# Kernel tuning notes

Hardware: AMD Instinct MI355X
Metric: run time of the kernel (lower is better)

## Reference

```python
import jax, jax.numpy as jnp
import numpy as np

N = 50000      # nodes
E = 800000     # edges (before self loops)
G = 64         # graphs in batch
F_IN = 11
HID = 64
C = 8
NEG_SLOPE = 0.2


def setup_inputs() -> dict:
    key = jax.random.key(0)
    ks = jax.random.split(key, 20)
    inp = {
        "x": jax.random.normal(ks[0], (N, F_IN), dtype=jnp.float32),
        "edge_index": jax.random.randint(ks[1], (2, E), 0, N, dtype=jnp.int64),
        "edge_attr": jax.random.normal(ks[2], (E, 17), dtype=jnp.float32),
        "batch": jnp.sort(jax.random.randint(ks[3], (N,), 0, G, dtype=jnp.int64)),
    }
    def glorot(k, shape):
        fan_in, fan_out = shape[0], shape[-1]
        s = jnp.sqrt(6.0 / (fan_in + fan_out))
        return jax.random.uniform(k, shape, jnp.float32, -s, s)
    # GATConv layers (heads=1): W [in,out], att vectors a_src/a_dst [out], bias [out]
    inp["W1"] = glorot(ks[4], (F_IN, HID)); inp["a1s"] = glorot(ks[5], (HID,)); inp["a1d"] = glorot(ks[6], (HID,)); inp["b1"] = jnp.zeros((HID,), jnp.float32)
    inp["W2"] = glorot(ks[7], (HID, HID)); inp["a2s"] = glorot(ks[8], (HID,)); inp["a2d"] = glorot(ks[9], (HID,)); inp["b2"] = jnp.zeros((HID,), jnp.float32)
    inp["W3"] = glorot(ks[10], (HID, C)); inp["a3s"] = glorot(ks[11], (C,)); inp["a3d"] = glorot(ks[12], (C,)); inp["b3"] = jnp.zeros((C,), jnp.float32)
    return inp


def _gat_layer(x, src, dst, W, a_s, a_d, b):
    # x: [N,in] -> h: [N,out]; single head, concat irrelevant for heads=1
    h = x @ W
    alpha_src = h @ a_s            # [N]
    alpha_dst = h @ a_d            # [N]
    e = jax.nn.leaky_relu(alpha_src[src] + alpha_dst[dst], negative_slope=NEG_SLOPE)  # [E']
    # segment-wise (per destination node) softmax over incoming edges
    m = jax.ops.segment_max(e, dst, num_segments=N)
    ex = jnp.exp(e - m[dst])
    denom = jax.ops.segment_sum(ex, dst, num_segments=N)
    alpha = ex / denom[dst]
    out = jax.ops.segment_sum(alpha[:, None] * h[src], dst, num_segments=N)
    return out + b


def reference(x, edge_index, edge_attr, batch, W1, a1s, a1d, b1, W2, a2s, a2d, b2, W3, a3s, a3d, b3):
    del edge_attr  # GATConv without edge_dim ignores edge_attr
    loop = jnp.arange(N, dtype=edge_index.dtype)
    src = jnp.concatenate([edge_index[0], loop])  # add self loops
    dst = jnp.concatenate([edge_index[1], loop])
    h = jax.nn.relu(_gat_layer(x, src, dst, W1, a1s, a1d, b1))
    h = jax.nn.relu(_gat_layer(h, src, dst, W2, a2s, a2d, b2))
    h = jax.nn.relu(_gat_layer(h, src, dst, W3, a3s, a3d, b3))
    # global mean pool over graphs
    counts = jax.ops.segment_sum(jnp.ones((N,), h.dtype), batch, num_segments=G)
    pooled = jax.ops.segment_sum(h, batch, num_segments=G) / jnp.maximum(counts, 1.0)[:, None]
    # dropout is identity in eval mode
    return jax.nn.sigmoid(pooled)
```

## Files before the change

kernel.cpp:

```cpp
#include <hip/hip_runtime.h>

#define NN 50000
#define EE 800000
#define GG 64
#define CC 8

#define NBKT 196
#define NCHK 782
#define CHUNK 1024
#define CAP 8192
#define NB4G 12500

__device__ unsigned g_done = 0;

__device__ __forceinline__ float lrelu(float z) { return fmaxf(z, 0.2f * z); }
__device__ __forceinline__ unsigned short f2bf(float v) {
    unsigned u = __float_as_uint(v);
    return (unsigned short)((u + 0x7FFFu + ((u >> 16) & 1u)) >> 16);
}
__device__ __forceinline__ float bf2f(unsigned short b) {
    return __uint_as_float(((unsigned)b) << 16);
}


__global__ __launch_bounds__(256) void k0_mm11_hist(const float* __restrict__ x, const float* __restrict__ W,
                                                    const float* __restrict__ avs, const float* __restrict__ avd,
                                                    unsigned short* __restrict__ h, float* __restrict__ as_,
                                                    float* __restrict__ ad_, const int* __restrict__ dst,
                                                    int* __restrict__ G) {
    __shared__ float xT[11 * 68];
    __shared__ float Wl[11 * 64];
    __shared__ float avl[64], adl[64];
    __shared__ int hist[NBKT];
    int t = threadIdx.x;
    int nbase = blockIdx.x * 64;
    for (int idx = t; idx < 11 * 64; idx += 256) Wl[idx] = W[idx];
    if (t < 64) { avl[t] = avs[t]; adl[t] = avd[t]; }
    for (int idx = t; idx < 64 * 11; idx += 256) {
        int n = idx / 11, k = idx - n * 11;
        int gn = nbase + n;
        if (gn >= NN) gn = NN - 1;
        xT[k * 68 + n] = x[gn * 11 + k];
    }
    for (int i = t; i < NBKT; i += 256) hist[i] = 0;
    __syncthreads();
    int f0 = (t & 15) * 4;
    int n0 = (t >> 4) * 4;
    float a00=0,a01=0,a02=0,a03=0, a10=0,a11=0,a12=0,a13=0;
    float a20=0,a21=0,a22=0,a23=0, a30=0,a31=0,a32=0,a33=0;
#pragma unroll
    for (int k = 0; k < 11; k++) {
        float4 xv = *(const float4*)&xT[k * 68 + n0];
        float4 wv = *(const float4*)&Wl[k * 64 + f0];
        a00 += xv.x * wv.x; a01 += xv.x * wv.y; a02 += xv.x * wv.z; a03 += xv.x * wv.w;
        a10 += xv.y * wv.x; a11 += xv.y * wv.y; a12 += xv.y * wv.z; a13 += xv.y * wv.w;
        a20 += xv.z * wv.x; a21 += xv.z * wv.y; a22 += xv.z * wv.z; a23 += xv.z * wv.w;
        a30 += xv.w * wv.x; a31 += xv.w * wv.y; a32 += xv.w * wv.z; a33 += xv.w * wv.w;
    }
    float4 av = *(const float4*)&avl[f0];
    float4 dv = *(const float4*)&adl[f0];
    float vs[4], vd[4];
    vs[0] = a00*av.x + a01*av.y + a02*av.z + a03*av.w;
    vs[1] = a10*av.x + a11*av.y + a12*av.z + a13*av.w;
    vs[2] = a20*av.x + a21*av.y + a22*av.z + a23*av.w;
    vs[3] = a30*av.x + a31*av.y + a32*av.z + a33*av.w;
    vd[0] = a00*dv.x + a01*dv.y + a02*dv.z + a03*dv.w;
    vd[1] = a10*dv.x + a11*dv.y + a12*dv.z + a13*dv.w;
    vd[2] = a20*dv.x + a21*dv.y + a22*dv.z + a23*dv.w;
    vd[3] = a30*dv.x + a31*dv.y + a32*dv.z + a33*dv.w;
#pragma unroll
    for (int o = 1; o < 16; o <<= 1) {
#pragma unroll
        for (int ni = 0; ni < 4; ni++) {
            vs[ni] += __shfl_xor(vs[ni], o);
            vd[ni] += __shfl_xor(vd[ni], o);
        }
    }
    ushort4* h4 = (ushort4*)h;
    int nn0 = nbase + n0;
    float rows[4][4] = {{a00,a01,a02,a03},{a10,a11,a12,a13},{a20,a21,a22,a23},{a30,a31,a32,a33}};
#pragma unroll
    for (int ni = 0; ni < 4; ni++) {
        if (nn0 + ni < NN) {
            ushort4 pv;
            pv.x = f2bf(rows[ni][0]); pv.y = f2bf(rows[ni][1]);
            pv.z = f2bf(rows[ni][2]); pv.w = f2bf(rows[ni][3]);
            h4[(nn0 + ni) * 16 + (t & 15)] = pv;
            if ((t & 15) == 0) { as_[nn0 + ni] = vs[ni]; ad_[nn0 + ni] = vd[ni]; }
        }
    }
    int e0 = blockIdx.x * CHUNK;
    int e1 = min(e0 + CHUNK, EE);
    for (int e = e0 + t; e < e1; e += 256) atomicAdd(&hist[dst[e] >> 8], 1);
    __syncthreads();
    for (int i = t; i < NBKT; i += 256) G[blockIdx.x * NBKT + i] = hist[i];
}


__global__ __launch_bounds__(256) void k1_scan(const int* __restrict__ G, int* __restrict__ offs,
                                               int* __restrict__ bT, float* __restrict__ pool,
                                               float* __restrict__ cntf, int* __restrict__ rowptr) {
    __shared__ int s[256];
    int t = threadIdx.x, j = blockIdx.x;
    int c0 = t * 4;
    int v0 = (c0 + 0 < NCHK) ? G[(c0 + 0) * NBKT + j] : 0;
    int v1 = (c0 + 1 < NCHK) ? G[(c0 + 1) * NBKT + j] : 0;
    int v2 = (c0 + 2 < NCHK) ? G[(c0 + 2) * NBKT + j] : 0;
    int v3 = (c0 + 3 < NCHK) ? G[(c0 + 3) * NBKT + j] : 0;
    int tsum = v0 + v1 + v2 + v3;
    s[t] = tsum;
    __syncthreads();
#pragma unroll
    for (int off = 1; off < 256; off <<= 1) {
        int u = (t >= off) ? s[t - off] : 0;
        __syncthreads();
        s[t] += u;
        __syncthreads();
    }
    int excl = s[t] - tsum;
    if (c0 + 0 < NCHK) offs[(c0 + 0) * NBKT + j] = excl;
    if (c0 + 1 < NCHK) offs[(c0 + 1) * NBKT + j] = excl + v0;
    if (c0 + 2 < NCHK) offs[(c0 + 2) * NBKT + j] = excl + v0 + v1;
    if (c0 + 3 < NCHK) offs[(c0 + 3) * NBKT + j] = excl + v0 + v1 + v2;
    if (t == 255) bT[j] = s[255];
    if (j == 0) {
        for (int i = t; i < GG * CC; i += 256) pool[i] = 0.f;
        if (t < GG) cntf[t] = 0.f;
        if (t == 0) rowptr[NN] = EE;
    }
}


__global__ __launch_bounds__(256) void k2_part(const int* __restrict__ src, const int* __restrict__ dst,
                                               const int* __restrict__ offs, const int* __restrict__ bT,
                                               unsigned* __restrict__ pairs) {
    __shared__ int s[256];
    __shared__ int bst[NBKT];
    __shared__ int cur[NBKT];
    int t = threadIdx.x, c = blockIdx.x;
    int v = (t < NBKT) ? bT[t] : 0;
    s[t] = v;
    __syncthreads();
#pragma unroll
    for (int off = 1; off < 256; off <<= 1) {
        int u = (t >= off) ? s[t - off] : 0;
        __syncthreads();
        s[t] += u;
        __syncthreads();
    }
    if (t < NBKT) bst[t] = s[t] - v;
    __syncthreads();
    for (int i = t; i < NBKT; i += 256) cur[i] = bst[i] + offs[c * NBKT + i];
    __syncthreads();
    int e0 = c * CHUNK, e1 = min(e0 + CHUNK, EE);
    for (int e = e0 + t; e < e1; e += 256) {
        int d = dst[e];
        int pos = atomicAdd(&cur[d >> 8], 1);
        pairs[pos] = (unsigned)src[e] | ((unsigned)(d & 255) << 16);
    }
}


__global__ __launch_bounds__(256) void k3_sort(const unsigned* __restrict__ pairs, const int* __restrict__ bT,
                                               int* __restrict__ col, int* __restrict__ rowptr) {
    __shared__ unsigned pL[CAP];
    __shared__ int hist[256];
    __shared__ int sc[256];
    int t = threadIdx.x, j = blockIdx.x;
    int v = (t < NBKT) ? bT[t] : 0;
    hist[t] = v;
    __syncthreads();
#pragma unroll
    for (int off = 1; off < 256; off <<= 1) {
        int u = (t >= off) ? hist[t - off] : 0;
        __syncthreads();
        hist[t] += u;
        __syncthreads();
    }
    if (t == j) { sc[0] = hist[t] - v; sc[1] = v; }
    __syncthreads();
    int start = sc[0];
    int cnt = sc[1];
    if (cnt > CAP) cnt = CAP;
    int nb = j * 256;
    int nodeCnt = min(256, NN - nb);
    __syncthreads();
    hist[t] = 0;
    __syncthreads();
    for (int i = t; i < cnt; i += 256) {
        unsigned p = pairs[start + i];
        pL[i] = p;
        atomicAdd(&hist[p >> 16], 1);
    }
    __syncthreads();
    int c2 = hist[t];
    sc[t] = c2;
    __syncthreads();
#pragma unroll
    for (int off = 1; off < 256; off <<= 1) {
        int u = (t >= off) ? sc[t - off] : 0;
        __syncthreads();
        sc[t] += u;
        __syncthreads();
    }
    int excl = sc[t] - c2;
    if (t < nodeCnt) rowptr[nb + t] = start + excl;
    hist[t] = excl;
    __syncthreads();
    for (int i = t; i < cnt; i += 256) {
        unsigned p = pL[i];
        int pos = atomicAdd(&hist[p >> 16], 1);
        col[start + pos] = (int)(p & 0xFFFFu);
    }
}


__global__ __launch_bounds__(256) void k_mm64t(const unsigned short* __restrict__ xin,
                                               const float* __restrict__ W,
                                               const float* __restrict__ avs, const float* __restrict__ avd,
                                               unsigned short* __restrict__ h, float* __restrict__ as_,
                                               float* __restrict__ ad_) {
    __shared__ float xT[64 * 68];
    __shared__ float Wl[64 * 64];
    __shared__ float avl[64], adl[64];
    int t = threadIdx.x;
    int nbase = blockIdx.x * 64;
    for (int idx = t; idx < 64 * 64; idx += 256) Wl[idx] = W[idx];
    if (t < 64) { avl[t] = avs[t]; adl[t] = avd[t]; }
    for (int idx = t; idx < 64 * 64; idx += 256) {
        int n = idx / 64, k = idx - n * 64;
        int gn = nbase + n;
        if (gn >= NN) gn = NN - 1;
        xT[k * 68 + n] = bf2f(xin[gn * 64 + k]);
    }
    __syncthreads();
    int f0 = (t & 15) * 4;
    int n0 = (t >> 4) * 4;
    float a00=0,a01=0,a02=0,a03=0, a10=0,a11=0,a12=0,a13=0;
    float a20=0,a21=0,a22=0,a23=0, a30=0,a31=0,a32=0,a33=0;
#pragma unroll 4
    for (int k = 0; k < 64; k++) {
        float4 xv = *(const float4*)&xT[k * 68 + n0];
        float4 wv = *(const float4*)&Wl[k * 64 + f0];
        a00 += xv.x * wv.x; a01 += xv.x * wv.y; a02 += xv.x * wv.z; a03 += xv.x * wv.w;
        a10 += xv.y * wv.x; a11 += xv.y * wv.y; a12 += xv.y * wv.z; a13 += xv.y * wv.w;
        a20 += xv.z * wv.x; a21 += xv.z * wv.y; a22 += xv.z * wv.z; a23 += xv.z * wv.w;
        a30 += xv.w * wv.x; a31 += xv.w * wv.y; a32 += xv.w * wv.z; a33 += xv.w * wv.w;
    }
    float4 av = *(const float4*)&avl[f0];
    float4 dv = *(const float4*)&adl[f0];
    float vs[4], vd[4];
    vs[0] = a00*av.x + a01*av.y + a02*av.z + a03*av.w;
    vs[1] = a10*av.x + a11*av.y + a12*av.z + a13*av.w;
    vs[2] = a20*av.x + a21*av.y + a22*av.z + a23*av.w;
    vs[3] = a30*av.x + a31*av.y + a32*av.z + a33*av.w;
    vd[0] = a00*dv.x + a01*dv.y + a02*dv.z + a03*dv.w;
    vd[1] = a10*dv.x + a11*dv.y + a12*dv.z + a13*dv.w;
    vd[2] = a20*dv.x + a21*dv.y + a22*dv.z + a23*dv.w;
    vd[3] = a30*dv.x + a31*dv.y + a32*dv.z + a33*dv.w;
#pragma unroll
    for (int o = 1; o < 16; o <<= 1) {
#pragma unroll
        for (int ni = 0; ni < 4; ni++) {
            vs[ni] += __shfl_xor(vs[ni], o);
            vd[ni] += __shfl_xor(vd[ni], o);
        }
    }
    ushort4* h4 = (ushort4*)h;
    int nn0 = nbase + n0;
    float rows[4][4] = {{a00,a01,a02,a03},{a10,a11,a12,a13},{a20,a21,a22,a23},{a30,a31,a32,a33}};
#pragma unroll
    for (int ni = 0; ni < 4; ni++) {
        if (nn0 + ni < NN) {
            ushort4 pv;
            pv.x = f2bf(rows[ni][0]); pv.y = f2bf(rows[ni][1]);
            pv.z = f2bf(rows[ni][2]); pv.w = f2bf(rows[ni][3]);
            h4[(nn0 + ni) * 16 + (t & 15)] = pv;
            if ((t & 15) == 0) { as_[nn0 + ni] = vs[ni]; ad_[nn0 + ni] = vd[ni]; }
        }
    }
}


template <bool FUSE>
__global__ __launch_bounds__(256) void k_agg64(const unsigned short* __restrict__ h,
                                               const int* __restrict__ rowptr,
                                               const int* __restrict__ col, const float* __restrict__ as_,
                                               const float* __restrict__ ad_, const float* __restrict__ bias,
                                               unsigned short* __restrict__ out16,
                                               const float* __restrict__ W3, const float* __restrict__ a3s,
                                               const float* __restrict__ a3d,
                                               float* __restrict__ as3, float* __restrict__ ad3) {
    __shared__ uint2 ws[4][64];
    __shared__ float W3p[64 * 10];
    if constexpr (FUSE) {
        for (int idx = threadIdx.x; idx < 512; idx += 256)
            W3p[(idx >> 3) * 10 + (idx & 7)] = W3[idx];
    }
    int wid = threadIdx.x >> 6;
    int node = blockIdx.x * 4 + wid;
    int lane = threadIdx.x & 63;
    int rp0 = rowptr[node];
    int deg = rowptr[node + 1] - rp0;
    float adn = ad_[node];
    float zself = lrelu(as_[node] + adn);
    const ushort4* hb = (const ushort4*)h;
    int f = lane & 15, eg = lane >> 4;
    float4 acc = make_float4(0.f, 0.f, 0.f, 0.f);
    if (deg <= 64) {
        int s = 0;
        float z = -1e30f;
        if (lane < deg) {
            s = col[rp0 + lane];
            z = lrelu(as_[s] + adn);
        }
        float M = z;
#pragma unroll
        for (int o = 32; o; o >>= 1) M = fmaxf(M, __shfl_xor(M, o));
        M = fmaxf(M, zself);
        float ex = (lane < deg) ? __expf(z - M) : 0.f;
        float exs = __expf(zself - M);
        float sum = ex;
#pragma unroll
        for (int o = 32; o; o >>= 1) sum += __shfl_xor(sum, o);
        float inv = 1.f / (sum + exs);
        float wl = ex * inv;
        ws[wid][lane] = make_uint2(__float_as_uint(wl), (unsigned)s);
        __syncthreads();
        const uint4* wsp = (const uint4*)&ws[wid][0];
        for (int base = 0; base < deg; base += 8) {
            uint4 p = wsp[(base >> 1) + eg];
            float wa = __uint_as_float(p.x);
            float wb = __uint_as_float(p.z);
            ushort4 ha = hb[p.y * 16 + f];
            ushort4 hc = hb[p.w * 16 + f];
            acc.x += wa * bf2f(ha.x) + wb * bf2f(hc.x);
            acc.y += wa * bf2f(ha.y) + wb * bf2f(hc.y);
            acc.z += wa * bf2f(ha.z) + wb * bf2f(hc.z);
            acc.w += wa * bf2f(ha.w) + wb * bf2f(hc.w);
        }
        if (eg == 0) {
            float w0 = exs * inv;
            ushort4 hv = hb[node * 16 + f];
            acc.x += w0 * bf2f(hv.x);
            acc.y += w0 * bf2f(hv.y);
            acc.z += w0 * bf2f(hv.z);
            acc.w += w0 * bf2f(hv.w);
        }
    } else {
        __syncthreads();
        float m = -1e30f, l = 0.f;
        for (int i = lane; i < deg; i += 64) {
            float z = lrelu(as_[col[rp0 + i]] + adn);
            float mn = fmaxf(m, z);
            l = l * __expf(m - mn) + __expf(z - mn);
            m = mn;
        }
        if (lane == 0) {
            float mn = fmaxf(m, zself);
            l = l * __expf(m - mn) + __expf(zself - mn);
            m = mn;
        }
#pragma unroll
        for (int o = 32; o; o >>= 1) {
            float mo = __shfl_xor(m, o), lo = __shfl_xor(l, o);
            float mn = fmaxf(m, mo);
            l = l * __expf(m - mn) + lo * __expf(mo - mn);
            m = mn;
        }
        float Em = m;
        float inv = 1.f / l;
        for (int base = 0; base < deg; base += 4) {
            int i = base + eg;
            if (i < deg) {
                int sv = col[rp0 + i];
                float al = __expf(lrelu(as_[sv] + adn) - Em) * inv;
                ushort4 hv = hb[sv * 16 + f];
                acc.x += al * bf2f(hv.x);
                acc.y += al * bf2f(hv.y);
                acc.z += al * bf2f(hv.z);
                acc.w += al * bf2f(hv.w);
            }
        }
        if (eg == 0) {
            float al = __expf(zself - Em) * inv;
            ushort4 hv = hb[node * 16 + f];
            acc.x += al * bf2f(hv.x);
            acc.y += al * bf2f(hv.y);
            acc.z += al * bf2f(hv.z);
            acc.w += al * bf2f(hv.w);
        }
    }
#pragma unroll
    for (int o = 16; o <= 32; o <<= 1) {
        acc.x += __shfl_xor(acc.x, o);
        acc.y += __shfl_xor(acc.y, o);
        acc.z += __shfl_xor(acc.z, o);
        acc.w += __shfl_xor(acc.w, o);
    }
    float4 bv = ((const float4*)bias)[f];
    float r0 = fmaxf(acc.x + bv.x, 0.f);
    float r1 = fmaxf(acc.y + bv.y, 0.f);
    float r2 = fmaxf(acc.z + bv.z, 0.f);
    float r3 = fmaxf(acc.w + bv.w, 0.f);
    if constexpr (!FUSE) {
        if (eg == 0) {
            ushort4 pv;
            pv.x = f2bf(r0); pv.y = f2bf(r1); pv.z = f2bf(r2); pv.w = f2bf(r3);
            ((ushort4*)out16)[node * 16 + f] = pv;
        }
    } else {
        int j0 = eg * 2;
        int kb = f * 4;
        float p0 = 0.f, p1 = 0.f;
#pragma unroll
        for (int i = 0; i < 4; i++) {
            float2 w = *(const float2*)&W3p[(kb + i) * 10 + j0];
            float rv = (i == 0) ? r0 : (i == 1) ? r1 : (i == 2) ? r2 : r3;
            p0 += rv * w.x;
            p1 += rv * w.y;
        }
#pragma unroll
        for (int o = 1; o < 16; o <<= 1) {
            p0 += __shfl_xor(p0, o);
            p1 += __shfl_xor(p1, o);
        }
        float vs = p0 * a3s[j0] + p1 * a3s[j0 + 1];
        float vd = p0 * a3d[j0] + p1 * a3d[j0 + 1];
        vs += __shfl_xor(vs, 16); vs += __shfl_xor(vs, 32);
        vd += __shfl_xor(vd, 16); vd += __shfl_xor(vd, 32);
        if (lane == 0) { as3[node] = vs; ad3[node] = vd; }
        if (f == 0) {
            ushort2 pv;
            pv.x = f2bf(p0); pv.y = f2bf(p1);
            ((ushort2*)out16)[node * 4 + eg] = pv;
        }
    }
}


__global__ __launch_bounds__(256) void k_agg8(const unsigned short* __restrict__ h,
                                              const int* __restrict__ rowptr,
                                              const int* __restrict__ col, const float* __restrict__ as_,
                                              const float* __restrict__ ad_, const float* __restrict__ bias,
                                              float* __restrict__ out) {
    __shared__ uint2 ws[4][64];
    int wid = threadIdx.x >> 6;
    int node = blockIdx.x * 4 + wid;
    int lane = threadIdx.x & 63;
    int rp0 = rowptr[node];
    int deg = rowptr[node + 1] - rp0;
    float adn = ad_[node];
    float zself = lrelu(as_[node] + adn);
    const ushort2* h2v = (const ushort2*)h;
    int f = lane & 3, eg = lane >> 2;
    float2 acc = make_float2(0.f, 0.f);
    if (deg <= 64) {
        int s = 0;
        float z = -1e30f;
        if (lane < deg) {
            s = col[rp0 + lane];
            z = lrelu(as_[s] + adn);
        }
        float M = z;
#pragma unroll
        for (int o = 32; o; o >>= 1) M = fmaxf(M, __shfl_xor(M, o));
        M = fmaxf(M, zself);
        float ex = (lane < deg) ? __expf(z - M) : 0.f;
        float exs = __expf(zself - M);
        float sum = ex;
#pragma unroll
        for (int o = 32; o; o >>= 1) sum += __shfl_xor(sum, o);
        float inv = 1.f / (sum + exs);
        float wl = ex * inv;
        ws[wid][lane] = make_uint2(__float_as_uint(wl), (unsigned)s);
        __syncthreads();
        const uint4* wsp = (const uint4*)&ws[wid][0];
        for (int base = 0; base < deg; base += 32) {
            uint4 p = wsp[(base >> 1) + eg];
            float wa = __uint_as_float(p.x);
            float wb = __uint_as_float(p.z);
            ushort2 ha = h2v[p.y * 4 + f];
            ushort2 hc = h2v[p.w * 4 + f];
            acc.x += wa * bf2f(ha.x) + wb * bf2f(hc.x);
            acc.y += wa * bf2f(ha.y) + wb * bf2f(hc.y);
        }
        if (eg == 0) {
            float w0 = exs * inv;
            ushort2 hv = h2v[node * 4 + f];
            acc.x += w0 * bf2f(hv.x);
            acc.y += w0 * bf2f(hv.y);
        }
    } else {
        __syncthreads();
        float m = -1e30f, l = 0.f;
        for (int i = lane; i < deg; i += 64) {
            float z = lrelu(as_[col[rp0 + i]] + adn);
            float mn = fmaxf(m, z);
            l = l * __expf(m - mn) + __expf(z - mn);
            m = mn;
        }
        if (lane == 0) {
            float mn = fmaxf(m, zself);
            l = l * __expf(m - mn) + __expf(zself - mn);
            m = mn;
        }
#pragma unroll
        for (int o = 32; o; o >>= 1) {
            float mo = __shfl_xor(m, o), lo = __shfl_xor(l, o);
            float mn = fmaxf(m, mo);
            l = l * __expf(m - mn) + lo * __expf(mo - mn);
            m = mn;
        }
        float Em = m;
        float inv = 1.f / l;
        for (int base = 0; base < deg; base += 16) {
            int i = base + eg;
            if (i < deg) {
                int sv = col[rp0 + i];
                float al = __expf(lrelu(as_[sv] + adn) - Em) * inv;
                ushort2 hv = h2v[sv * 4 + f];
                acc.x += al * bf2f(hv.x);
                acc.y += al * bf2f(hv.y);
            }
        }
        if (eg == 0) {
            float al = __expf(zself - Em) * inv;
            ushort2 hv = h2v[node * 4 + f];
            acc.x += al * bf2f(hv.x);
            acc.y += al * bf2f(hv.y);
        }
    }
#pragma unroll
    for (int o = 4; o <= 32; o <<= 1) {
        acc.x += __shfl_xor(acc.x, o);
        acc.y += __shfl_xor(acc.y, o);
    }
    if (eg == 0) {
        float2 bv = ((const float2*)bias)[f];
        float2 o2;
        o2.x = fmaxf(acc.x + bv.x, 0.f);
        o2.y = fmaxf(acc.y + bv.y, 0.f);
        ((float2*)out)[node * 4 + f] = o2;
    }
}


__global__ __launch_bounds__(256) void k9_poolfinal(const float* __restrict__ h3, const int* __restrict__ batch,
                                                    float* __restrict__ pool, float* __restrict__ cntf,
                                                    float* __restrict__ out) {
    __shared__ float pl[GG * CC + GG];
    __shared__ int lastFlag;
    int t = threadIdx.x;
    for (int idx = t; idx < GG * CC + GG; idx += 256) pl[idx] = 0.f;
    __syncthreads();
    int node = blockIdx.x * 256 + t;
    if (node < NN) {
        int g = batch[node];
#pragma unroll
        for (int c = 0; c < CC; c++) atomicAdd(&pl[g * CC + c], h3[node * CC + c]);
        atomicAdd(&pl[GG * CC + g], 1.0f);
    }
    __syncthreads();
    for (int idx = t; idx < GG * CC + GG; idx += 256) {
        float v = pl[idx];
        if (idx < GG * CC)
            atomicAdd(&pool[idx], v);
        else
            atomicAdd(&cntf[idx - GG * CC], v);
    }
    __syncthreads();
    if (t == 0) {
        __threadfence();
        unsigned r = __hip_atomic_fetch_add(&g_done, 1u, __ATOMIC_ACQ_REL, __HIP_MEMORY_SCOPE_AGENT);
        lastFlag = (r == (unsigned)(NBKT - 1));
    }
    __syncthreads();
    if (lastFlag) {
        __threadfence();
        for (int i = t; i < GG * CC; i += 256) {
            int g = i >> 3;
            float c = __hip_atomic_load(&cntf[g], __ATOMIC_RELAXED, __HIP_MEMORY_SCOPE_AGENT);
            float p = __hip_atomic_load(&pool[i], __ATOMIC_RELAXED, __HIP_MEMORY_SCOPE_AGENT);
            float v = p / fmaxf(c, 1.0f);
            out[i] = 1.0f / (1.0f + __expf(-v));
        }
        if (t == 0)
            __hip_atomic_store(&g_done, 0u, __ATOMIC_RELAXED, __HIP_MEMORY_SCOPE_AGENT);
    }
}


extern "C" void kernel_launch(void* const* d_in, const int* in_sizes, int n_in,
                              void* d_out, int out_size, void* d_ws, size_t ws_size,
                              hipStream_t stream) {
    const float* x   = (const float*)d_in[0];
    const int*   ei  = (const int*)d_in[1];
    const int*   bat = (const int*)d_in[3];
    const float* W1  = (const float*)d_in[4];
    const float* a1s = (const float*)d_in[5];
    const float* a1d = (const float*)d_in[6];
    const float* b1  = (const float*)d_in[7];
    const float* W2  = (const float*)d_in[8];
    const float* a2s = (const float*)d_in[9];
    const float* a2d = (const float*)d_in[10];
    const float* b2  = (const float*)d_in[11];
    const float* W3  = (const float*)d_in[12];
    const float* a3s = (const float*)d_in[13];
    const float* a3d = (const float*)d_in[14];
    const float* b3  = (const float*)d_in[15];
    float* out = (float*)d_out;

    float* fb = (float*)d_ws;
    unsigned short* hA16 = (unsigned short*)fb;
    unsigned short* hB16 = (unsigned short*)(fb + NN * 32);
    unsigned short* h316 = (unsigned short*)(fb + NN * 64);
    float* h3b  = fb + NN * 64 + NN * 4;
    float* as_  = h3b + NN * 8;
    float* ad_  = as_ + NN;
    float* as3  = ad_ + NN;
    float* ad3  = as3 + NN;
    int* rowptr = (int*)(ad3 + NN);
    int* col    = rowptr + NN + 1;
    int* G      = col + EE;
    int* offs   = G + NCHK * NBKT;
    int* bT     = offs + NCHK * NBKT;
    unsigned* pairs = (unsigned*)(bT + 256);
    float* pool = (float*)(pairs + EE);
    float* cntf = pool + GG * CC;

    const int NB64 = (NN + 63) / 64;

    const int* srcE = ei;
    const int* dstE = ei + EE;

    k0_mm11_hist<<<NB64, 256, 0, stream>>>(x, W1, a1s, a1d, hA16, as_, ad_, dstE, G);
    k1_scan<<<NBKT, 256, 0, stream>>>(G, offs, bT, pool, cntf, rowptr);
    k2_part<<<NCHK, 256, 0, stream>>>(srcE, dstE, offs, bT, pairs);
    k3_sort<<<NBKT, 256, 0, stream>>>(pairs, bT, col, rowptr);

    k_agg64<false><<<NB4G, 256, 0, stream>>>(hA16, rowptr, col, as_, ad_, b1, hB16,
                                             nullptr, nullptr, nullptr, nullptr, nullptr);
    k_mm64t<<<NB64, 256, 0, stream>>>(hB16, W2, a2s, a2d, hA16, as_, ad_);
    k_agg64<true><<<NB4G, 256, 0, stream>>>(hA16, rowptr, col, as_, ad_, b2, h316,
                                            W3, a3s, a3d, as3, ad3);
    k_agg8<<<NB4G, 256, 0, stream>>>(h316, rowptr, col, as3, ad3, b3, h3b);
    k9_poolfinal<<<NBKT, 256, 0, stream>>>(h3b, bat, pool, cntf, out);
}
```

Baseline: 271.3 us.

## Prefetch neighbor feature rows into registers before softmax in GAT aggregation

For nodes with degree at most 64, the aggregation kernels now issue all neighbor feature gathers into a register array before computing the softmax max and sum. Each edge's weight is then fetched by shuffle instead of going through a shared-memory staging buffer guarded by a block barrier. This lets gather latency overlap with the softmax reductions and removes the __syncthreads from the hot path. It also unpacks bf16 pairs from 32-bit words, and the cost is more registers per thread, 16 uint2 in the 64-wide kernel, which may lower occupancy.

```diff
diff --git a/kernel.cpp b/kernel.cpp
--- a/kernel.cpp
+++ b/kernel.cpp
@@ -20,6 +20,12 @@
 }
 __device__ __forceinline__ float bf2f(unsigned short b) {
     return __uint_as_float(((unsigned)b) << 16);
+}
+__device__ __forceinline__ float2 bf2x2(unsigned d) {
+    float2 r;
+    r.x = __uint_as_float(d << 16);
+    r.y = __uint_as_float(d & 0xFFFF0000u);
+    return r;
 }
 
 
@@ -291,11 +297,11 @@
                                                const float* __restrict__ W3, const float* __restrict__ a3s,
                                                const float* __restrict__ a3d,
                                                float* __restrict__ as3, float* __restrict__ ad3) {
-    __shared__ uint2 ws[4][64];
     __shared__ float W3p[64 * 10];
     if constexpr (FUSE) {
         for (int idx = threadIdx.x; idx < 512; idx += 256)
             W3p[(idx >> 3) * 10 + (idx & 7)] = W3[idx];
+        __syncthreads();
     }
     int wid = threadIdx.x >> 6;
     int node = blockIdx.x * 4 + wid;
@@ -304,7 +310,7 @@
     int deg = rowptr[node + 1] - rp0;
     float adn = ad_[node];
     float zself = lrelu(as_[node] + adn);
-    const ushort4* hb = (const ushort4*)h;
+    const uint2* hb2 = (const uint2*)h;
     int f = lane & 15, eg = lane >> 4;
     float4 acc = make_float4(0.f, 0.f, 0.f, 0.f);
     if (deg <= 64) {
@@ -314,6 +320,17 @@
             s = col[rp0 + lane];
             z = lrelu(as_[s] + adn);
         }
+        uint2 rowreg[16];
+#pragma unroll
+        for (int k = 0; k < 16; k++) {
+            int e = k * 4 + eg;
+            uint2 r = make_uint2(0u, 0u);
+            if (e < deg) {
+                int se = __shfl(s, e);
+                r = hb2[se * 16 + f];
+            }
+            rowreg[k] = r;
+        }
         float M = z;
 #pragma unroll
         for (int o = 32; o; o >>= 1) M = fmaxf(M, __shfl_xor(M, o));
@@ -325,30 +342,30 @@
         for (int o = 32; o; o >>= 1) sum += __shfl_xor(sum, o);
         float inv = 1.f / (sum + exs);
         float wl = ex * inv;
-        ws[wid][lane] = make_uint2(__float_as_uint(wl), (unsigned)s);
-        __syncthreads();
-        const uint4* wsp = (const uint4*)&ws[wid][0];
-        for (int base = 0; base < deg; base += 8) {
-            uint4 p = wsp[(base >> 1) + eg];
-            float wa = __uint_as_float(p.x);
-            float wb = __uint_as_float(p.z);
-            ushort4 ha = hb[p.y * 16 + f];
-            ushort4 hc = hb[p.w * 16 + f];
-            acc.x += wa * bf2f(ha.x) + wb * bf2f(hc.x);
-            acc.y += wa * bf2f(ha.y) + wb * bf2f(hc.y);
-            acc.z += wa * bf2f(ha.z) + wb * bf2f(hc.z);
-            acc.w += wa * bf2f(ha.w) + wb * bf2f(hc.w);
+#pragma unroll
+        for (int k = 0; k < 16; k++) {
+            int e = k * 4 + eg;
+            if (e < deg) {
+                float w = __shfl(wl, e);
+                float2 lo = bf2x2(rowreg[k].x);
+                float2 hi = bf2x2(rowreg[k].y);
+                acc.x += w * lo.x;
+                acc.y += w * lo.y;
+                acc.z += w * hi.x;
+                acc.w += w * hi.y;
+            }
         }
         if (eg == 0) {
             float w0 = exs * inv;
-            ushort4 hv = hb[node * 16 + f];
-            acc.x += w0 * bf2f(hv.x);
-            acc.y += w0 * bf2f(hv.y);
-            acc.z += w0 * bf2f(hv.z);
-            acc.w += w0 * bf2f(hv.w);
+            uint2 hv = hb2[node * 16 + f];
+            float2 lo = bf2x2(hv.x);
+            float2 hi = bf2x2(hv.y);
+            acc.x += w0 * lo.x;
+            acc.y += w0 * lo.y;
+            acc.z += w0 * hi.x;
+            acc.w += w0 * hi.y;
         }
     } else {
-        __syncthreads();
         float m = -1e30f, l = 0.f;
         for (int i = lane; i < deg; i += 64) {
             float z = lrelu(as_[col[rp0 + i]] + adn);
@@ -375,20 +392,24 @@
             if (i < deg) {
                 int sv = col[rp0 + i];
                 float al = __expf(lrelu(as_[sv] + adn) - Em) * inv;
-                ushort4 hv = hb[sv * 16 + f];
-                acc.x += al * bf2f(hv.x);
-                acc.y += al * bf2f(hv.y);
-                acc.z += al * bf2f(hv.z);
-                acc.w += al * bf2f(hv.w);
+                uint2 hv = hb2[sv * 16 + f];
+                float2 lo = bf2x2(hv.x);
+                float2 hi = bf2x2(hv.y);
+                acc.x += al * lo.x;
+                acc.y += al * lo.y;
+                acc.z += al * hi.x;
+                acc.w += al * hi.y;
             }
         }
         if (eg == 0) {
             float al = __expf(zself - Em) * inv;
-            ushort4 hv = hb[node * 16 + f];
-            acc.x += al * bf2f(hv.x);
-            acc.y += al * bf2f(hv.y);
-            acc.z += al * bf2f(hv.z);
-            acc.w += al * bf2f(hv.w);
+            uint2 hv = hb2[node * 16 + f];
+            float2 lo = bf2x2(hv.x);
+            float2 hi = bf2x2(hv.y);
+            acc.x += al * lo.x;
+            acc.y += al * lo.y;
+            acc.z += al * hi.x;
+            acc.w += al * hi.y;
         }
     }
 #pragma unroll
@@ -444,7 +465,6 @@
                                               const int* __restrict__ col, const float* __restrict__ as_,
                                               const float* __restrict__ ad_, const float* __restrict__ bias,
                                               float* __restrict__ out) {
-    __shared__ uint2 ws[4][64];
     int wid = threadIdx.x >> 6;
     int node = blockIdx.x * 4 + wid;
     int lane = threadIdx.x & 63;
@@ -452,7 +472,7 @@
     int deg = rowptr[node + 1] - rp0;
     float adn = ad_[node];
     float zself = lrelu(as_[node] + adn);
-    const ushort2* h2v = (const ushort2*)h;
+    const unsigned* h1 = (const unsigned*)h;
     int f = lane & 3, eg = lane >> 2;
     float2 acc = make_float2(0.f, 0.f);
     if (deg <= 64) {
@@ -462,6 +482,17 @@
             s = col[rp0 + lane];
             z = lrelu(as_[s] + adn);
         }
+        unsigned rowreg[4];
+#pragma unroll
+        for (int k = 0; k < 4; k++) {
+            int e = k * 16 + eg;
+            unsigned r = 0u;
+            if (e < deg) {
+                int se = __shfl(s, e);
+                r = h1[se * 4 + f];
+            }
+            rowreg[k] = r;
+        }
         float M = z;
 #pragma unroll
         for (int o = 32; o; o >>= 1) M = fmaxf(M, __shfl_xor(M, o));
@@ -473,26 +504,23 @@
         for (int o = 32; o; o >>= 1) sum += __shfl_xor(sum, o);
         float inv = 1.f / (sum + exs);
         float wl = ex * inv;
-        ws[wid][lane] = make_uint2(__float_as_uint(wl), (unsigned)s);
-        __syncthreads();
-        const uint4* wsp = (const uint4*)&ws[wid][0];
-        for (int base = 0; base < deg; base += 32) {
-            uint4 p = wsp[(base >> 1) + eg];
-            float wa = __uint_as_float(p.x);
-            float wb = __uint_as_float(p.z);
-            ushort2 ha = h2v[p.y * 4 + f];
-            ushort2 hc = h2v[p.w * 4 + f];
-            acc.x += wa * bf2f(ha.x) + wb * bf2f(hc.x);
-            acc.y += wa * bf2f(ha.y) + wb * bf2f(hc.y);
+#pragma unroll
+        for (int k = 0; k < 4; k++) {
+            int e = k * 16 + eg;
+            if (e < deg) {
+                float w = __shfl(wl, e);
+                float2 hv = bf2x2(rowreg[k]);
+                acc.x += w * hv.x;
+                acc.y += w * hv.y;
+            }
         }
         if (eg == 0) {
             float w0 = exs * inv;
-            ushort2 hv = h2v[node * 4 + f];
-            acc.x += w0 * bf2f(hv.x);
-            acc.y += w0 * bf2f(hv.y);
+            float2 hv = bf2x2(h1[node * 4 + f]);
+            acc.x += w0 * hv.x;
+            acc.y += w0 * hv.y;
         }
     } else {
-        __syncthreads();
         float m = -1e30f, l = 0.f;
         for (int i = lane; i < deg; i += 64) {
             float z = lrelu(as_[col[rp0 + i]] + adn);
@@ -519,16 +547,16 @@
             if (i < deg) {
                 int sv = col[rp0 + i];
                 float al = __expf(lrelu(as_[sv] + adn) - Em) * inv;
-                ushort2 hv = h2v[sv * 4 + f];
-                acc.x += al * bf2f(hv.x);
-                acc.y += al * bf2f(hv.y);
+                float2 hv = bf2x2(h1[sv * 4 + f]);
+                acc.x += al * hv.x;
+                acc.y += al * hv.y;
             }
         }
         if (eg == 0) {
             float al = __expf(zself - Em) * inv;
-            ushort2 hv = h2v[node * 4 + f];
-            acc.x += al * bf2f(hv.x);
-            acc.y += al * bf2f(hv.y);
+            float2 hv = bf2x2(h1[node * 4 + f]);
+            acc.x += al * hv.x;
+            acc.y += al * hv.y;
         }
     }
 #pragma unroll
```

New measurement: 270.2 us. Within noise of the previous version (-0.4%).
